# Performance work log

Hardware: AMD Instinct MI355X
Metric: run time of the kernel (lower is better)

The kernel has to match this reference:

```python
import jax, jax.numpy as jnp
import numpy as np

DIMS = [1024, 2048, 2048, 51]
B, P = 16, 1024


def setup_inputs() -> dict:
    key = jax.random.key(0)
    ks = jax.random.split(key, 1 + 2 * (len(DIMS) - 1))
    inp = {
        "num_pairs": P,
        "classifier_input": jax.random.normal(ks[0], (B, P, DIMS[0]), dtype=jnp.float32),
        "num_batches": B,
    }
    # Linear params, PyTorch-style: W[out, in], b[out]
    for li in range(len(DIMS) - 1):
        fan_in = DIMS[li]
        bound = 1.0 / np.sqrt(fan_in)
        inp[f"W{li}"] = jax.random.uniform(ks[1 + 2 * li], (DIMS[li + 1], fan_in), minval=-bound, maxval=bound, dtype=jnp.float32)
        inp[f"b{li}"] = jax.random.uniform(ks[2 + 2 * li], (DIMS[li + 1],), minval=-bound, maxval=bound, dtype=jnp.float32)
    return inp


def reference(num_pairs, classifier_input, num_batches, W0, b0, W1, b1, W2, b2):
    # Batched MLP over all (num_batches * num_pairs) vectors at once.
    # Original loops per (b, i); math is identical. dropout p=0.0 -> identity.
    x = classifier_input  # [B, P, d_in]
    x = jax.nn.relu(jnp.einsum("bpd,hd->bph", x, W0) + b0)
    x = jax.nn.relu(jnp.einsum("bpd,hd->bph", x, W1) + b1)
    out = jnp.einsum("bpd,od->bpo", x, W2) + b2  # [B, P, n_classes]
    return out
```

## Files before the change

kernel.cpp:

```cpp
#include <hip/hip_runtime.h>
#include <hip/hip_bf16.h>
#include <stdint.h>

typedef __attribute__((ext_vector_type(8))) short short8;
typedef __attribute__((ext_vector_type(8))) uint16_t ushort8;
typedef __attribute__((ext_vector_type(4))) float floatx4;

#define TK 64


__device__ __forceinline__ uint16_t f2bf_bits(float f) {
    uint32_t u = __builtin_bit_cast(uint32_t, f);
    u += 0x7FFFu + ((u >> 16) & 1u);
    return (uint16_t)(u >> 16);
}

__device__ __forceinline__ void async_copy16(const void* g, void* l) {
    auto gp = (const __attribute__((address_space(1))) uint32_t*)(uintptr_t)g;
    auto lp = (__attribute__((address_space(3))) uint32_t*)(uint32_t)(uintptr_t)l;
    __builtin_amdgcn_global_load_lds(gp, lp, 16, 0, 0);
}


__global__ void cvt8(const float* __restrict__ src, uint16_t* __restrict__ dst, int n) {
    int i = (blockIdx.x * 256 + threadIdx.x) * 8;
    if (i >= n) return;
    floatx4 a = *(const floatx4*)(src + i);
    floatx4 b = *(const floatx4*)(src + i + 4);
    ushort8 o;
#pragma unroll
    for (int k = 0; k < 4; k++) {
        o[k]     = f2bf_bits(a[k]);
        o[k + 4] = f2bf_bits(b[k]);
    }
    *(ushort8*)(dst + i) = o;
}

__global__ void cvt_pad_w2(const float* __restrict__ src, uint16_t* __restrict__ dst) {
    int i = (blockIdx.x * 256 + threadIdx.x) * 8;
    int row = i >> 11;
    ushort8 o;
    if (row < 51) {
        floatx4 a = *(const floatx4*)(src + i);
        floatx4 b = *(const floatx4*)(src + i + 4);
#pragma unroll
        for (int k = 0; k < 4; k++) {
            o[k]     = f2bf_bits(a[k]);
            o[k + 4] = f2bf_bits(b[k]);
        }
    } else {
#pragma unroll
        for (int k = 0; k < 8; k++) o[k] = 0;
    }
    *(ushort8*)(dst + i) = o;
}


template <int MI, int NJ, bool RELU, bool OUTF32>
__global__ __launch_bounds__(256, 2)
void gemm_bt(const uint16_t* __restrict__ A,
             const uint16_t* __restrict__ W,
             const float* __restrict__ bias,
             void* __restrict__ out,
             int M, int N, int K, int ldc, int nstore)
{
    constexpr int TMv = MI * 32;
    constexpr int TNv = NJ * 32;
    constexpr int ACH = TMv / 32;
    constexpr int BCH = TNv / 32;

    __shared__ alignas(16) uint16_t sA[TMv * TK];
    __shared__ alignas(16) uint16_t sB[TNv * TK];

    const int tid  = threadIdx.x;
    const int wave = tid >> 6;
    const int lane = tid & 63;

    const int f   = blockIdx.x;
    const int xcd = f & 7;
    const int loc = f >> 3;
    const int per = (int)gridDim.x >> 3;
    const int nt  = N / TNv;
    const int n_t = loc % nt;
    const int m_t = xcd * (per / nt) + loc / nt;
    const int n0 = n_t * TNv;
    const int m0 = m_t * TMv;

    floatx4 acc[MI][NJ];
    const floatx4 zero = {0.f, 0.f, 0.f, 0.f};
#pragma unroll
    for (int i = 0; i < MI; i++)
#pragma unroll
        for (int j = 0; j < NJ; j++) acc[i][j] = zero;

    const int wr = (wave >> 1) * MI * 16;
    const int wc = (wave & 1) * NJ * 16;

    const int sr   = lane >> 3;
    const int scol = ((lane & 7) ^ sr) * 8;

    const uint16_t* ap[ACH];
    const uint16_t* bp[BCH];
#pragma unroll
    for (int t = 0; t < ACH; t++)
        ap[t] = A + (size_t)(m0 + (wave + 4 * t) * 8 + sr) * K + scol;
#pragma unroll
    for (int t = 0; t < BCH; t++)
        bp[t] = W + (size_t)(n0 + (wave + 4 * t) * 8 + sr) * K + scol;

    const int fm = lane & 15;
    const int fr = fm & 7;
    const int kgb = lane >> 4;

    const int niter = K / TK;
    for (int it = 0; it < niter; it++) {
#pragma unroll
        for (int t = 0; t < ACH; t++) {
            async_copy16(ap[t], sA + (wave + 4 * t) * 512);
            ap[t] += TK;
        }
#pragma unroll
        for (int t = 0; t < BCH; t++) {
            async_copy16(bp[t], sB + (wave + 4 * t) * 512);
            bp[t] += TK;
        }
        __syncthreads();

#pragma unroll
        for (int kk = 0; kk < 2; kk++) {
            const int slot = ((kgb + 4 * kk) ^ fr) * 8;
            short8 af[MI], bfr[NJ];
#pragma unroll
            for (int i = 0; i < MI; i++)
                af[i] = *(const short8*)(sA + (wr + i * 16 + fm) * TK + slot);
#pragma unroll
            for (int j = 0; j < NJ; j++)
                bfr[j] = *(const short8*)(sB + (wc + j * 16 + fm) * TK + slot);
#pragma unroll
            for (int i = 0; i < MI; i++)
#pragma unroll
                for (int j = 0; j < NJ; j++)
                    acc[i][j] = __builtin_amdgcn_mfma_f32_16x16x32_bf16(af[i], bfr[j], acc[i][j], 0, 0, 0);
        }
        __syncthreads();
    }

    const int cr = (lane >> 4) * 4;
    const int cc = lane & 15;
#pragma unroll
    for (int i = 0; i < MI; i++) {
        const int gmb = m0 + wr + i * 16 + cr;
#pragma unroll
        for (int j = 0; j < NJ; j++) {
            const int gn = n0 + wc + j * 16 + cc;
            if (gn < nstore) {
                const float bv = bias[gn];
#pragma unroll
                for (int r = 0; r < 4; r++) {
                    float v = acc[i][j][r] + bv;
                    if (RELU) v = fmaxf(v, 0.f);
                    const size_t idx = (size_t)(gmb + r) * ldc + gn;
                    if (OUTF32) ((float*)out)[idx] = v;
                    else        ((uint16_t*)out)[idx] = f2bf_bits(v);
                }
            }
        }
    }
}


#define PH_PRE(QM, QN, SA, SB) \
    short8 af[4][2], bf[2][2]; \
    { const uint16_t* sAq = (SA) + (QM) * 8192 + aoff; \
      const uint16_t* sBq = (SB) + (QN) * 8192 + boff; \
      _Pragma("unroll") \
      for (int kk = 0; kk < 2; kk++) { \
        const int sl = ((kgb + 4 * kk) ^ fr) * 8; \
        _Pragma("unroll") \
        for (int mi = 0; mi < 4; mi++) af[mi][kk] = *(const short8*)(sAq + mi * 1024 + sl); \
        _Pragma("unroll") \
        for (int nj = 0; nj < 2; nj++) bf[nj][kk] = *(const short8*)(sBq + nj * 1024 + sl); \
      } }

#define PH_POST(QM, QN) \
    __builtin_amdgcn_sched_barrier(0); \
    __builtin_amdgcn_s_barrier(); \
    asm volatile("s_waitcnt lgkmcnt(0)" ::: "memory"); \
    __builtin_amdgcn_sched_barrier(0); \
    __builtin_amdgcn_s_setprio(1); \
    _Pragma("unroll") \
    for (int kk = 0; kk < 2; kk++) \
      _Pragma("unroll") \
      for (int mi = 0; mi < 4; mi++) \
        _Pragma("unroll") \
        for (int nj = 0; nj < 2; nj++) \
          acc[QM][QN][mi][nj] = __builtin_amdgcn_mfma_f32_16x16x32_bf16( \
              af[mi][kk], bf[nj][kk], acc[QM][QN][mi][nj], 0, 0, 0); \
    __builtin_amdgcn_s_setprio(0); \
    __builtin_amdgcn_sched_barrier(0); \
    __builtin_amdgcn_s_barrier(); \
    __builtin_amdgcn_sched_barrier(0);

template <bool RELU, bool OUTF32>
__global__ __launch_bounds__(512, 2)
void gemm256(const uint16_t* __restrict__ A,
             const uint16_t* __restrict__ W,
             const float* __restrict__ bias,
             void* __restrict__ out,
             int K, int N, int ldc, int nstore)
{
    extern __shared__ uint16_t smem[];
    uint16_t* sA0 = smem;
    uint16_t* sA1 = smem + 16384;
    uint16_t* sB0 = smem + 32768;
    uint16_t* sB1 = smem + 49152;

    const int tid  = threadIdx.x;
    const int wave = tid >> 6;
    const int lane = tid & 63;
    const int wm2  = wave >> 2;
    const int wn2  = wave & 3;

    const int f   = blockIdx.x;
    const int xcd = f & 7;
    const int loc = f >> 3;
    const int per = (int)gridDim.x >> 3;
    const int ntn = N / 256;
    const int n_t = loc % ntn;
    const int m_t = xcd * (per / ntn) + loc / ntn;
    const int m0 = m_t * 256;
    const int n0 = n_t * 256;

    floatx4 acc[2][2][4][2];
    const floatx4 zero = {0.f, 0.f, 0.f, 0.f};
#pragma unroll
    for (int qm = 0; qm < 2; qm++)
#pragma unroll
    for (int qn = 0; qn < 2; qn++)
#pragma unroll
    for (int mi = 0; mi < 4; mi++)
#pragma unroll
    for (int nj = 0; nj < 2; nj++) acc[qm][qn][mi][nj] = zero;

    const int srow = lane >> 3;
    const int scol = ((lane & 7) ^ srow) * 8;
    const uint16_t* pA = A + (size_t)(m0 + wave * 8 + srow) * K + scol;
    const uint16_t* pB = W + (size_t)(n0 + wave * 8 + srow) * K + scol;

    auto stA = [&](int h, int kt, uint16_t* buf) {
        const uint16_t* p = pA + (size_t)h * 128 * K + (size_t)kt * 64;
        async_copy16(p,                 buf + h * 8192 + wave * 512);
        async_copy16(p + (size_t)64 * K, buf + h * 8192 + 4096 + wave * 512);
    };
    auto stB = [&](int h, int kt, uint16_t* buf) {
        const uint16_t* p = pB + (size_t)h * 128 * K + (size_t)kt * 64;
        async_copy16(p,                 buf + h * 8192 + wave * 512);
        async_copy16(p + (size_t)64 * K, buf + h * 8192 + 4096 + wave * 512);
    };

    const int fm  = lane & 15;
    const int fr  = fm & 7;
    const int kgb = lane >> 4;
    const int aoff = (wm2 * 64 + fm) * 64;
    const int boff = (wn2 * 32 + fm) * 64;

    stA(0, 0, sA0);
    stB(0, 0, sB0);
    stA(1, 0, sA0);
    stB(1, 0, sB0);
    stA(0, 1, sA1);
    stB(1, 1, sB1);
    asm volatile("s_waitcnt vmcnt(4)" ::: "memory");
    __builtin_amdgcn_s_barrier();
    __builtin_amdgcn_sched_barrier(0);

    const int niter2 = K / 128;
    for (int it = 0; it < niter2; ++it) {
        const int T = 2 * it;
        const bool last = (it == niter2 - 1);

        { PH_PRE(0, 0, sA0, sB0);
          stB(0, T + 1, sB1);
          asm volatile("s_waitcnt lgkmcnt(8)");
          PH_POST(0, 0); }

        { PH_PRE(0, 1, sA0, sB0);
          stA(1, T + 1, sA1);
          asm volatile("s_waitcnt lgkmcnt(8)");
          PH_POST(0, 1); }

        { PH_PRE(1, 1, sA0, sB0);
          if (!last) stA(0, T + 2, sA0);
          asm volatile("s_waitcnt lgkmcnt(8)");
          PH_POST(1, 1); }

        { PH_PRE(1, 0, sA0, sB0);
          if (!last) stB(1, T + 2, sB0);
          asm volatile("s_waitcnt lgkmcnt(8)");
          if (last) asm volatile("s_waitcnt vmcnt(0)" ::: "memory");
          else      asm volatile("s_waitcnt vmcnt(4)" ::: "memory");
          PH_POST(1, 0); }

        { PH_PRE(0, 0, sA1, sB1);
          if (!last) stB(0, T + 2, sB0);
          asm volatile("s_waitcnt lgkmcnt(8)");
          PH_POST(0, 0); }

        { PH_PRE(0, 1, sA1, sB1);
          if (!last) stA(1, T + 2, sA0);
          asm volatile("s_waitcnt lgkmcnt(8)");
          PH_POST(0, 1); }

        { PH_PRE(1, 1, sA1, sB1);
          if (!last) stA(0, T + 3, sA1);
          asm volatile("s_waitcnt lgkmcnt(8)");
          PH_POST(1, 1); }

        { PH_PRE(1, 0, sA1, sB1);
          if (!last) {
            stB(1, T + 3, sB1);
            asm volatile("s_waitcnt lgkmcnt(8)");
            asm volatile("s_waitcnt vmcnt(4)" ::: "memory");
          }
          PH_POST(1, 0); }
    }

    const int cr = (lane >> 4) * 4;
    const int cc = lane & 15;
#pragma unroll
    for (int qm = 0; qm < 2; qm++)
#pragma unroll
    for (int mi = 0; mi < 4; mi++) {
        const int gm = m0 + qm * 128 + wm2 * 64 + mi * 16 + cr;
#pragma unroll
        for (int qn = 0; qn < 2; qn++)
#pragma unroll
        for (int nj = 0; nj < 2; nj++) {
            const int gn = n0 + qn * 128 + wn2 * 32 + nj * 16 + cc;
            if (gn < nstore) {
                const float bv = bias[gn];
#pragma unroll
                for (int r = 0; r < 4; r++) {
                    float v = acc[qm][qn][mi][nj][r] + bv;
                    if (RELU) v = fmaxf(v, 0.f);
                    const size_t idx = (size_t)(gm + r) * ldc + gn;
                    if (OUTF32) ((float*)out)[idx] = v;
                    else        ((uint16_t*)out)[idx] = f2bf_bits(v);
                }
            }
        }
    }
}


extern "C" void kernel_launch(void* const* d_in, const int* in_sizes, int n_in,
                              void* d_out, int out_size, void* d_ws, size_t ws_size,
                              hipStream_t stream) {
    (void)in_sizes; (void)n_in; (void)out_size; (void)ws_size;
    const float* X  = (const float*)d_in[1];
    const float* W0 = (const float*)d_in[3];
    const float* b0 = (const float*)d_in[4];
    const float* W1 = (const float*)d_in[5];
    const float* b1 = (const float*)d_in[6];
    const float* W2 = (const float*)d_in[7];
    const float* b2 = (const float*)d_in[8];

    const int M = 16384;

    static bool attr_done = false;
    if (!attr_done) {
        (void)hipFuncSetAttribute((const void*)gemm256<true, false>,
                                  hipFuncAttributeMaxDynamicSharedMemorySize, 131072);
        attr_done = true;
    }

    char* w = (char*)d_ws;
    uint16_t* X0  = (uint16_t*)w; w += (size_t)M * 1024 * 2;
    uint16_t* X1  = (uint16_t*)w; w += (size_t)M * 2048 * 2;
    uint16_t* X2  = (uint16_t*)w; w += (size_t)M * 2048 * 2;
    uint16_t* W0b = (uint16_t*)w; w += (size_t)2048 * 1024 * 2;
    uint16_t* W1b = (uint16_t*)w; w += (size_t)2048 * 2048 * 2;
    uint16_t* W2b = (uint16_t*)w; w += (size_t)64 * 2048 * 2;

    cvt8<<<M * 1024 / 8 / 256, 256, 0, stream>>>(X, X0, M * 1024);
    cvt8<<<2048 * 1024 / 8 / 256, 256, 0, stream>>>(W0, W0b, 2048 * 1024);
    cvt8<<<2048 * 2048 / 8 / 256, 256, 0, stream>>>(W1, W1b, 2048 * 2048);
    cvt_pad_w2<<<64 * 2048 / 8 / 256, 256, 0, stream>>>(W2, W2b);

    gemm256<true, false><<<dim3((M / 256) * (2048 / 256)), 512, 131072, stream>>>(
        X0, W0b, b0, X1, 1024, 2048, 2048, 2048);
    gemm256<true, false><<<dim3((M / 256) * (2048 / 256)), 512, 131072, stream>>>(
        X1, W1b, b1, X2, 2048, 2048, 2048, 2048);
    gemm_bt<1, 2, false, true><<<dim3(M / 32), 256, 0, stream>>>(
        X2, W2b, b2, d_out, M, 64, 2048, 51, 51);
}
```

Before: 369.7 us.

## Reuse A/B LDS fragments across sub-tiles and restructure prefetch schedule

Splits the per-phase fragment loads into separate A and B loads held in registers (af, b0, b1). Each phase now reloads only the operand that changed between consecutive sub-tiles, using a snake order (0,0)->(0,1)->(1,1)->(1,0). This cuts LDS read traffic per K-step. The global-to-LDS prefetch order and vmcnt thresholds are rearranged to match, and the last iteration is peeled out of the loop. It adds register pressure from holding two B fragment sets, and the reworked waitcnt logic risks hazards on buffer reuse.

```diff
diff --git a/kernel.cpp b/kernel.cpp
--- a/kernel.cpp
+++ b/kernel.cpp
@@ -169,24 +169,33 @@
 }
 
 
-#define PH_PRE(QM, QN, SA, SB) \
-    short8 af[4][2], bf[2][2]; \
-    { const uint16_t* sAq = (SA) + (QM) * 8192 + aoff; \
-      const uint16_t* sBq = (SB) + (QN) * 8192 + boff; \
+#define SCHED0 __builtin_amdgcn_sched_barrier(0)
+
+#define LOAD_A(SA, QM) do { \
+    const uint16_t* _p = (SA) + (QM) * 8192 + aoff; \
+    _Pragma("unroll") \
+    for (int kk = 0; kk < 2; kk++) { \
+      const int sl = ((kgb + 4 * kk) ^ fr) * 8; \
       _Pragma("unroll") \
-      for (int kk = 0; kk < 2; kk++) { \
-        const int sl = ((kgb + 4 * kk) ^ fr) * 8; \
-        _Pragma("unroll") \
-        for (int mi = 0; mi < 4; mi++) af[mi][kk] = *(const short8*)(sAq + mi * 1024 + sl); \
-        _Pragma("unroll") \
-        for (int nj = 0; nj < 2; nj++) bf[nj][kk] = *(const short8*)(sBq + nj * 1024 + sl); \
-      } }
-
-#define PH_POST(QM, QN) \
-    __builtin_amdgcn_sched_barrier(0); \
+      for (int mi = 0; mi < 4; mi++) \
+        af[mi][kk] = *(const short8*)(_p + mi * 1024 + sl); \
+    } } while (0)
+
+#define LOAD_B(SB, QN, BF) do { \
+    const uint16_t* _p = (SB) + (QN) * 8192 + boff; \
+    _Pragma("unroll") \
+    for (int kk = 0; kk < 2; kk++) { \
+      const int sl = ((kgb + 4 * kk) ^ fr) * 8; \
+      _Pragma("unroll") \
+      for (int nj = 0; nj < 2; nj++) \
+        BF[nj][kk] = *(const short8*)(_p + nj * 1024 + sl); \
+    } } while (0)
+
+#define PH_MFMA(QM, QN, BF) \
+    SCHED0; \
     __builtin_amdgcn_s_barrier(); \
     asm volatile("s_waitcnt lgkmcnt(0)" ::: "memory"); \
-    __builtin_amdgcn_sched_barrier(0); \
+    SCHED0; \
     __builtin_amdgcn_s_setprio(1); \
     _Pragma("unroll") \
     for (int kk = 0; kk < 2; kk++) \
@@ -195,11 +204,55 @@
         _Pragma("unroll") \
         for (int nj = 0; nj < 2; nj++) \
           acc[QM][QN][mi][nj] = __builtin_amdgcn_mfma_f32_16x16x32_bf16( \
-              af[mi][kk], bf[nj][kk], acc[QM][QN][mi][nj], 0, 0, 0); \
+              af[mi][kk], BF[nj][kk], acc[QM][QN][mi][nj], 0, 0, 0); \
     __builtin_amdgcn_s_setprio(0); \
-    __builtin_amdgcn_sched_barrier(0); \
+    SCHED0; \
     __builtin_amdgcn_s_barrier(); \
-    __builtin_amdgcn_sched_barrier(0);
+    SCHED0;
+
+#define ITER_BODY(T, LAST) \
+     \
+    LOAD_A(sA0, 0); \
+    LOAD_B(sB0, 0, b0); \
+    stA(1, (T) + 1, sA1); \
+    asm volatile("s_waitcnt lgkmcnt(8)"); \
+    PH_MFMA(0, 0, b0); \
+     \
+    LOAD_B(sB0, 1, b1); \
+    if (!(LAST)) stA(0, (T) + 2, sA0); \
+    PH_MFMA(0, 1, b1); \
+     \
+    LOAD_A(sA0, 1); \
+    if (!(LAST)) stB(0, (T) + 2, sB0); \
+    PH_MFMA(1, 1, b1); \
+     \
+    if (!(LAST)) { \
+      stB(1, (T) + 2, sB0); \
+      asm volatile("s_waitcnt vmcnt(6)" ::: "memory"); \
+    } else { \
+      asm volatile("s_waitcnt vmcnt(0)" ::: "memory"); \
+    } \
+    PH_MFMA(1, 0, b0); \
+     \
+    LOAD_A(sA1, 0); \
+    LOAD_B(sB1, 0, b0); \
+    if (!(LAST)) stA(1, (T) + 2, sA0); \
+    asm volatile("s_waitcnt lgkmcnt(8)"); \
+    PH_MFMA(0, 0, b0); \
+     \
+    LOAD_B(sB1, 1, b1); \
+    if (!(LAST)) stA(0, (T) + 3, sA1); \
+    PH_MFMA(0, 1, b1); \
+     \
+    LOAD_A(sA1, 1); \
+    if (!(LAST)) stB(0, (T) + 3, sB1); \
+    PH_MFMA(1, 1, b1); \
+     \
+    if (!(LAST)) { \
+      stB(1, (T) + 3, sB1); \
+      asm volatile("s_waitcnt vmcnt(6)" ::: "memory"); \
+    } \
+    PH_MFMA(1, 0, b0);
 
 template <bool RELU, bool OUTF32>
 __global__ __launch_bounds__(512, 2)
@@ -249,12 +302,12 @@
 
     auto stA = [&](int h, int kt, uint16_t* buf) {
         const uint16_t* p = pA + (size_t)h * 128 * K + (size_t)kt * 64;
-        async_copy16(p,                 buf + h * 8192 + wave * 512);
+        async_copy16(p,                  buf + h * 8192 + wave * 512);
         async_copy16(p + (size_t)64 * K, buf + h * 8192 + 4096 + wave * 512);
     };
     auto stB = [&](int h, int kt, uint16_t* buf) {
         const uint16_t* p = pB + (size_t)h * 128 * K + (size_t)kt * 64;
-        async_copy16(p,                 buf + h * 8192 + wave * 512);
+        async_copy16(p,                  buf + h * 8192 + wave * 512);
         async_copy16(p + (size_t)64 * K, buf + h * 8192 + 4096 + wave * 512);
     };
 
@@ -264,65 +317,29 @@
     const int aoff = (wm2 * 64 + fm) * 64;
     const int boff = (wn2 * 32 + fm) * 64;
 
+    short8 af[4][2];
+    short8 b0[2][2];
+    short8 b1[2][2];
+
     stA(0, 0, sA0);
     stB(0, 0, sB0);
     stA(1, 0, sA0);
     stB(1, 0, sB0);
     stA(0, 1, sA1);
+    stB(0, 1, sB1);
     stB(1, 1, sB1);
-    asm volatile("s_waitcnt vmcnt(4)" ::: "memory");
+    asm volatile("s_waitcnt vmcnt(6)" ::: "memory");
     __builtin_amdgcn_s_barrier();
-    __builtin_amdgcn_sched_barrier(0);
+    SCHED0;
 
     const int niter2 = K / 128;
-    for (int it = 0; it < niter2; ++it) {
+    for (int it = 0; it < niter2 - 1; ++it) {
         const int T = 2 * it;
-        const bool last = (it == niter2 - 1);
-
-        { PH_PRE(0, 0, sA0, sB0);
-          stB(0, T + 1, sB1);
-          asm volatile("s_waitcnt lgkmcnt(8)");
-          PH_POST(0, 0); }
-
-        { PH_PRE(0, 1, sA0, sB0);
-          stA(1, T + 1, sA1);
-          asm volatile("s_waitcnt lgkmcnt(8)");
-          PH_POST(0, 1); }
-
-        { PH_PRE(1, 1, sA0, sB0);
-          if (!last) stA(0, T + 2, sA0);
-          asm volatile("s_waitcnt lgkmcnt(8)");
-          PH_POST(1, 1); }
-
-        { PH_PRE(1, 0, sA0, sB0);
-          if (!last) stB(1, T + 2, sB0);
-          asm volatile("s_waitcnt lgkmcnt(8)");
-          if (last) asm volatile("s_waitcnt vmcnt(0)" ::: "memory");
-          else      asm volatile("s_waitcnt vmcnt(4)" ::: "memory");
-          PH_POST(1, 0); }
-
-        { PH_PRE(0, 0, sA1, sB1);
-          if (!last) stB(0, T + 2, sB0);
-          asm volatile("s_waitcnt lgkmcnt(8)");
-          PH_POST(0, 0); }
-
-        { PH_PRE(0, 1, sA1, sB1);
-          if (!last) stA(1, T + 2, sA0);
-          asm volatile("s_waitcnt lgkmcnt(8)");
-          PH_POST(0, 1); }
-
-        { PH_PRE(1, 1, sA1, sB1);
-          if (!last) stA(0, T + 3, sA1);
-          asm volatile("s_waitcnt lgkmcnt(8)");
-          PH_POST(1, 1); }
-
-        { PH_PRE(1, 0, sA1, sB1);
-          if (!last) {
-            stB(1, T + 3, sB1);
-            asm volatile("s_waitcnt lgkmcnt(8)");
-            asm volatile("s_waitcnt vmcnt(4)" ::: "memory");
-          }
-          PH_POST(1, 0); }
+        ITER_BODY(T, false);
+    }
+    {
+        const int T = 2 * (niter2 - 1);
+        ITER_BODY(T, true);
     }
 
     const int cr = (lane >> 4) * 4;
```

Measured after the change: 349.1 us. 1.06x faster.
